# Kernel optimization log

Measured on AMD Instinct MI355X. Metric: run time of the kernel, lower is better.

## Reference

```python
import jax, jax.numpy as jnp
import numpy as np

D_MODEL = 1024
NUM_HEADS = 16
HEAD_SIZE = D_MODEL // NUM_HEADS  # 64; used ONLY as the softmax scale (module never splits heads)


def setup_inputs() -> dict:
    key = jax.random.key(0)
    ks = jax.random.split(key, 7)
    B, L, D = 4, 2048, D_MODEL
    q = jax.random.normal(ks[0], (B, L, D), dtype=jnp.float32)
    k = jax.random.normal(ks[1], (B, L, D), dtype=jnp.float32)
    v = jax.random.normal(ks[2], (B, L, D), dtype=jnp.float32)
    s = 1.0 / np.sqrt(D)
    Wq = jax.random.uniform(ks[3], (D, D), jnp.float32, -s, s)
    Wk = jax.random.uniform(ks[4], (D, D), jnp.float32, -s, s)
    Wv = jax.random.uniform(ks[5], (D, D), jnp.float32, -s, s)
    Wproj = jax.random.uniform(ks[6], (D, D), jnp.float32, -s, s)
    return {"q": q, "k": k, "v": v, "Wq": Wq, "Wk": Wk, "Wv": Wv, "Wproj": Wproj}


def reference(q, k, v, Wq, Wk, Wv, Wproj):
    # nn.Linear(x) = x @ W.T; weights stored [out, in]
    L = q.shape[1]
    qh = jnp.einsum('bld,ed->ble', q, Wq)
    kh = jnp.einsum('bld,ed->ble', k, Wk)
    vh = jnp.einsum('bld,ed->ble', v, Wv)
    # NOTE: module attends over the full d_model channel (no head split),
    # but scales by head_size ** -0.5 — faithful to the source.
    att = jnp.einsum('bqd,bkd->bqk', qh, kh) * (HEAD_SIZE ** -0.5)
    causal = jnp.tril(jnp.ones((L, L), dtype=bool))  # bias buffer
    att = jnp.where(causal, att, -jnp.inf)
    att = jax.nn.softmax(att, axis=-1)
    y = jnp.einsum('bqk,bkd->bqd', att, vh)
    y = jnp.einsum('bld,ed->ble', y, Wproj)
    return y
```

## Files before the change

kernel.cpp:

```cpp
#include <hip/hip_runtime.h>
#include <hip/hip_bf16.h>
#include <stdint.h>

typedef __bf16 bf16x8 __attribute__((ext_vector_type(8)));
typedef float  f32x4  __attribute__((ext_vector_type(4)));
typedef unsigned short ushort8v __attribute__((ext_vector_type(8)));

__device__ __forceinline__ unsigned short f2bf(float f) {
  unsigned int u = __float_as_uint(f);
  u += 0x7FFF + ((u >> 16) & 1);
  return (unsigned short)(u >> 16);
}
__device__ __forceinline__ float bf2f(unsigned short h) {
  return __uint_as_float(((unsigned int)h) << 16);
}

#define GLOAD_LDS(gptr, ldsptr)                                                     \
  __builtin_amdgcn_global_load_lds(                                                 \
      (const __attribute__((address_space(1))) unsigned int*)(gptr),                \
      (__attribute__((address_space(3))) unsigned int*)(ldsptr), 16, 0, 0)

__global__ __launch_bounds__(512, 1) void gemm8p(
    const unsigned short* __restrict__ A,
    const unsigned short* __restrict__ B,
    void* __restrict__ C,
    int M, int N, int K, int ntn,
    long sAz, long sBz, long sCz,
    int mode, int tilemap, float scale)
{
  int mt, nt;
  const int orig = blockIdx.x;
  if (tilemap == 0) {
    const int nwg = gridDim.x;
    const int qq = nwg >> 3, rr = nwg & 7, xcd = orig & 7, oo = orig >> 3;
    const int wg = (xcd < rr ? xcd * (qq + 1) : rr * (qq + 1) + (xcd - rr) * qq) + oo;
    mt = wg / ntn; nt = wg % ntn;
  } else {
    mt = (int)((sqrtf(8.f * orig + 1.f) - 1.f) * 0.5f);
    int base = mt * (mt + 1) / 2;
    if (orig < base) { mt--; base = mt * (mt + 1) / 2; }
    else if (orig >= base + mt + 1) { mt++; base = mt * (mt + 1) / 2; }
    nt = orig - base;
  }
  const int z = blockIdx.y;
  A += sAz * (long)z;
  B += sBz * (long)z;

  __shared__ __align__(16) unsigned short lds[65536];

  const int tid  = threadIdx.x;
  const int wave = tid >> 6;
  const int lane = tid & 63;
  const int wr = wave >> 2, wc = wave & 3;
  const int li = lane & 15;
  const int rslot = (((lane >> 4) ^ ((lane >> 1) & 3)) << 4);

  f32x4 acc[8][4];
#pragma unroll
  for (int i = 0; i < 8; ++i)
#pragma unroll
    for (int j = 0; j < 4; ++j) acc[i][j] = (f32x4){0.f, 0.f, 0.f, 0.f};

  const int nkt = K / 64;

  const int srow = tid >> 2;
  const long scol = (long)(((tid & 3) ^ ((tid >> 3) & 3)) << 3);
  const long aoff0 = (long)(mt * 256 + srow) * K + scol;
  const long aoff1 = (long)(mt * 256 + 128 + srow) * K + scol;
  const long boff0 = (long)(nt * 256 + srow) * K + scol;
  const long boff1 = (long)(nt * 256 + 128 + srow) * K + scol;
  const int stw = wave * 1024;

#define AB(c, kh) (((c) * 2 + (kh)) * 16384)
#define BB(c, kh) (65536 + ((c) * 2 + (kh)) * 16384)
#define STAGE_A(c, kh, jt) do { const long o_ = (long)(jt) * 64 + (kh) * 32;        \
    GLOAD_LDS(A + aoff0 + o_, (char*)lds + AB(c, kh) + stw);                        \
    GLOAD_LDS(A + aoff1 + o_, (char*)lds + AB(c, kh) + 8192 + stw); } while (0)
#define STAGE_B(c, kh, jt) do { const long o_ = (long)(jt) * 64 + (kh) * 32;        \
    GLOAD_LDS(B + boff0 + o_, (char*)lds + BB(c, kh) + stw);                        \
    GLOAD_LDS(B + boff1 + o_, (char*)lds + BB(c, kh) + 8192 + stw); } while (0)
#define RD_A(c, kk, ms, mf) \
  (*(const bf16x8*)((const char*)lds + AB(c, kk) + (wr * 128 + (ms) * 64 + (mf) * 16 + li) * 64 + rslot))
#define RD_B(c, kk, nf) \
  (*(const bf16x8*)((const char*)lds + BB(c, kk) + (wc * 64 + (nf) * 16 + li) * 64 + rslot))
#define MM(msb, bb) do {                                                            \
    _Pragma("unroll")                                                               \
    for (int mf_ = 0; mf_ < 4; ++mf_)                                               \
    _Pragma("unroll")                                                               \
      for (int nf_ = 0; nf_ < 4; ++nf_)                                             \
        acc[(msb) + mf_][nf_] = __builtin_amdgcn_mfma_f32_16x16x32_bf16(            \
            a[mf_], bb[nf_], acc[(msb) + mf_][nf_], 0, 0, 0); } while (0)
#define LGKM0_FENCE do {                                                            \
    asm volatile("s_waitcnt lgkmcnt(0)" ::: "memory");                              \
    __builtin_amdgcn_sched_barrier(0); } while (0)
#define BARRIER do { __builtin_amdgcn_s_barrier();                                  \
    asm volatile("" ::: "memory"); } while (0)

  STAGE_A(0, 0, 0); STAGE_B(0, 0, 0); STAGE_A(0, 1, 0); STAGE_B(0, 1, 0);
  asm volatile("s_waitcnt vmcnt(0)" ::: "memory");
  BARRIER;

  bf16x8 a[4], b0[4], b1[4];
  for (int j = 0; j < nkt; ++j) {
    const int c = j & 1;
    const bool s1 = (j + 1 < nkt);

#pragma unroll
    for (int nf = 0; nf < 4; ++nf) b0[nf] = RD_B(c, 0, nf);
#pragma unroll
    for (int mf = 0; mf < 4; ++mf) a[mf] = RD_A(c, 0, 0, mf);
    if (s1) STAGE_A(c ^ 1, 0, j + 1);
    BARRIER;
    LGKM0_FENCE;
    __builtin_amdgcn_s_setprio(1);
    MM(0, b0);
    __builtin_amdgcn_s_setprio(0);
    BARRIER;

#pragma unroll
    for (int mf = 0; mf < 4; ++mf) a[mf] = RD_A(c, 0, 1, mf);
    if (s1) STAGE_B(c ^ 1, 0, j + 1);
    BARRIER;
    LGKM0_FENCE;
    __builtin_amdgcn_s_setprio(1);
    MM(4, b0);
    __builtin_amdgcn_s_setprio(0);
    if (s1) { asm volatile("s_waitcnt vmcnt(4)" ::: "memory"); }
    else    { asm volatile("s_waitcnt vmcnt(0)" ::: "memory"); }
    BARRIER;

#pragma unroll
    for (int nf = 0; nf < 4; ++nf) b1[nf] = RD_B(c, 1, nf);
#pragma unroll
    for (int mf = 0; mf < 4; ++mf) a[mf] = RD_A(c, 1, 0, mf);
    if (s1) STAGE_A(c ^ 1, 1, j + 1);
    BARRIER;
    LGKM0_FENCE;
    __builtin_amdgcn_s_setprio(1);
    MM(0, b1);
    __builtin_amdgcn_s_setprio(0);
    BARRIER;

#pragma unroll
    for (int mf = 0; mf < 4; ++mf) a[mf] = RD_A(c, 1, 1, mf);
    if (s1) STAGE_B(c ^ 1, 1, j + 1);
    BARRIER;
    LGKM0_FENCE;
    __builtin_amdgcn_s_setprio(1);
    MM(4, b1);
    __builtin_amdgcn_s_setprio(0);
    if (s1) { asm volatile("s_waitcnt vmcnt(4)" ::: "memory"); }
    BARRIER;
  }
#undef AB
#undef BB
#undef STAGE_A
#undef STAGE_B
#undef RD_A
#undef RD_B
#undef MM
#undef LGKM0_FENCE
#undef BARRIER

  const int rb = mt * 256 + wr * 128;
  const int cb = nt * 256 + wc * 64;
  unsigned short* Cb = (unsigned short*)C + sCz * (long)z;
#pragma unroll
  for (int mi = 0; mi < 8; ++mi)
#pragma unroll
    for (int ni = 0; ni < 4; ++ni) {
      const int row0 = rb + mi * 16 + ((lane >> 4) << 2);
      const int col  = cb + ni * 16 + (lane & 15);
#pragma unroll
      for (int jj = 0; jj < 4; ++jj)
        Cb[(long)(row0 + jj) * N + col] = f2bf(acc[mi][ni][jj] * scale);
    }
}

#define BM 128
#define BN 128
#define BK 32

__global__ __launch_bounds__(256, 3) void gemm_bt(
    const unsigned short* __restrict__ A,
    const unsigned short* __restrict__ B,
    void* __restrict__ C,
    int M, int N, int K, int ntiles,
    long sAz, long sBz, long sCz,
    int mode, int tilemap, float scale)
{
  int mt, nt;
  const int orig = blockIdx.x;
  if (tilemap == 0) {
    const int nwg = gridDim.x;
    const int qq = nwg >> 3, rr = nwg & 7, xc = orig & 7, oo = orig >> 3;
    const int wg = (xc < rr ? xc * (qq + 1) : rr * (qq + 1) + (xc - rr) * qq) + oo;
    mt = wg / ntiles; nt = wg % ntiles;
  } else {
    const int c = orig & 15;
    mt = (c & 8) ? (15 - (c & 7)) : c;
    nt = orig >> 4;
  }
  const int z = blockIdx.y;
  const int emode = (mode == 3) ? (z == 2 ? 1 : 0) : mode;

  A += sAz * (long)z;
  B += sBz * (long)z;

  __shared__ __align__(16) unsigned short As[3][BM * BK];
  __shared__ __align__(16) unsigned short Bs[3][BN * BK];

  const int tid  = threadIdx.x;
  const int wave = tid >> 6;
  const int lane = tid & 63;
  const int wr = wave >> 1, wc = wave & 1;

  f32x4 acc[4][4];
#pragma unroll
  for (int i = 0; i < 4; ++i)
#pragma unroll
    for (int j = 0; j < 4; ++j) acc[i][j] = (f32x4){0.f, 0.f, 0.f, 0.f};

  int kiters = K / BK;
  if (tilemap == 2) { const int kl = (mt + 1) * (BM / BK); if (kl < kiters) kiters = kl; }

  const int r0 = tid >> 2, s0 = tid & 3;
  const int c0 = ((s0 ^ ((r0 >> 1) & 3)) << 3);
  const int r1 = r0 + 64;
  const int c1 = ((s0 ^ ((r1 >> 1) & 3)) << 3);
  const long aoff0 = (long)(mt * BM + r0) * K + c0;
  const long aoff1 = (long)(mt * BM + r1) * K + c1;
  const long boff0 = (long)(nt * BN + r0) * K + c0;
  const long boff1 = (long)(nt * BN + r1) * K + c1;
  const unsigned ldsw = wave * 1024;

#define STAGE(bi, k0)                                                     \
  do {                                                                    \
    GLOAD_LDS(A + aoff0 + (k0), (char*)&As[bi][0]    + ldsw);             \
    GLOAD_LDS(A + aoff1 + (k0), (char*)&As[bi][2048] + ldsw);             \
    GLOAD_LDS(B + boff0 + (k0), (char*)&Bs[bi][0]    + ldsw);             \
    GLOAD_LDS(B + boff1 + (k0), (char*)&Bs[bi][2048] + ldsw);             \
  } while (0)

  STAGE(0, 0);
  if (kiters > 1) STAGE(1, BK);

  int cur = 0;
  for (int kt = 0; kt < kiters; ++kt) {
    const int rem = kiters - 1 - kt;
    if (rem >= 2) {
      int sb = cur + 2; if (sb >= 3) sb -= 3;
      STAGE(sb, (kt + 2) * BK);
      asm volatile("s_waitcnt vmcnt(8)" ::: "memory");
    } else if (rem == 1) {
      asm volatile("s_waitcnt vmcnt(4)" ::: "memory");
    } else {
      asm volatile("s_waitcnt vmcnt(0)" ::: "memory");
    }
    __builtin_amdgcn_s_barrier();
    asm volatile("" ::: "memory");

    bf16x8 af[4], bfr[4];
#pragma unroll
    for (int i = 0; i < 4; ++i) {
      const int ar = wr * 64 + i * 16 + (lane & 15);
      const int as = ((lane >> 4) ^ ((ar >> 1) & 3)) << 3;
      af[i] = *(const bf16x8*)&As[cur][ar * BK + as];
      const int br = wc * 64 + i * 16 + (lane & 15);
      const int bs = ((lane >> 4) ^ ((br >> 1) & 3)) << 3;
      bfr[i] = *(const bf16x8*)&Bs[cur][br * BK + bs];
    }
#pragma unroll
    for (int mi = 0; mi < 4; ++mi)
#pragma unroll
      for (int ni = 0; ni < 4; ++ni)
        acc[mi][ni] = __builtin_amdgcn_mfma_f32_16x16x32_bf16(af[mi], bfr[ni], acc[mi][ni], 0, 0, 0);

    asm volatile("" ::: "memory");
    __builtin_amdgcn_s_barrier();
    cur = (cur == 2) ? 0 : cur + 1;
  }
#undef STAGE

  const int rb = mt * BM + wr * 64;
  const int cb = nt * BN + wc * 64;

  if (emode == 0) {
    unsigned short* Cb = (unsigned short*)C + sCz * (long)z;
#pragma unroll
    for (int mi = 0; mi < 4; ++mi)
#pragma unroll
      for (int ni = 0; ni < 4; ++ni) {
        const int row0 = rb + mi * 16 + ((lane >> 4) << 2);
        const int col  = cb + ni * 16 + (lane & 15);
#pragma unroll
        for (int j = 0; j < 4; ++j)
          Cb[(long)(row0 + j) * N + col] = f2bf(acc[mi][ni][j] * scale);
      }
  } else if (emode == 1) {
    unsigned short* Cb = (unsigned short*)C + sCz * (long)z;
#pragma unroll
    for (int mi = 0; mi < 4; ++mi)
#pragma unroll
      for (int ni = 0; ni < 4; ++ni) {
        const int row0 = rb + mi * 16 + ((lane >> 4) << 2);
        const int col  = cb + ni * 16 + (lane & 15);
#pragma unroll
        for (int j = 0; j < 4; ++j) {
          const int row = row0 + j;
          const int b = row >> 11, l = row & 2047;
          Cb[((long)b * N + col) * 2048 + l] = f2bf(acc[mi][ni][j]);
        }
      }
  } else {
    float* Cf = (float*)C + sCz * (long)z;
#pragma unroll
    for (int mi = 0; mi < 4; ++mi)
#pragma unroll
      for (int ni = 0; ni < 4; ++ni) {
        const int row0 = rb + mi * 16 + ((lane >> 4) << 2);
        const int col  = cb + ni * 16 + (lane & 15);
#pragma unroll
        for (int j = 0; j < 4; ++j)
          Cf[(long)(row0 + j) * N + col] = acc[mi][ni][j] * scale;
      }
  }
}

__global__ __launch_bounds__(256) void softmax_causal(
    const unsigned short* __restrict__ S, unsigned short* __restrict__ P)
{
  const int r = blockIdx.x;
  const int b = r >> 11, q = r & 2047;
  const unsigned short* srow = S + ((long)b * 2048 + q) * 2048;
  unsigned short* prow = P + ((long)b * 2048 + q) * 2048;
  const int len = q + 1;
  const int lenceil = ((q >> 7) + 1) << 7;
  const int tid = threadIdx.x, lane = tid & 63, wave = tid >> 6;
  const int base = tid * 8;
  const bool active = base < lenceil;
  __shared__ float red[8];

  float vv[8];
#pragma unroll
  for (int i = 0; i < 8; ++i) vv[i] = -3.4e38f;
  if (active) {
    ushort8v xv = *(const ushort8v*)(srow + base);
#pragma unroll
    for (int i = 0; i < 8; ++i) vv[i] = bf2f(xv[i]);
  }

  float m = -3.4e38f;
#pragma unroll
  for (int i = 0; i < 8; ++i) if (base + i < len) m = fmaxf(m, vv[i]);
#pragma unroll
  for (int o = 32; o; o >>= 1) m = fmaxf(m, __shfl_xor(m, o));
  if (lane == 0) red[wave] = m;
  __syncthreads();
  m = fmaxf(fmaxf(red[0], red[1]), fmaxf(red[2], red[3]));

  float p[8], s = 0.f;
#pragma unroll
  for (int i = 0; i < 8; ++i) {
    p[i] = (base + i < len) ? __expf(vv[i] - m) : 0.f;
    s += p[i];
  }
#pragma unroll
  for (int o = 32; o; o >>= 1) s += __shfl_xor(s, o);
  if (lane == 0) red[4 + wave] = s;
  __syncthreads();
  s = (red[4] + red[5]) + (red[6] + red[7]);
  const float inv = 1.f / s;

  if (active) {
    ushort8v o16;
#pragma unroll
    for (int i = 0; i < 8; ++i) o16[i] = f2bf(p[i] * inv);
    *(ushort8v*)(prow + base) = o16;
  }
}

__global__ __launch_bounds__(256) void convert_all(
    const float* __restrict__ q, const float* __restrict__ k, const float* __restrict__ v,
    const float* __restrict__ wq, const float* __restrict__ wk,
    const float* __restrict__ wv, const float* __restrict__ wp,
    unsigned short* __restrict__ qkv, unsigned short* __restrict__ wb)
{
  const long NQ = 8192L * 1024 / 4;
  const long NW = 1024L * 1024 / 4;
  const int blk = blockIdx.x;
  const float* src; unsigned short* dst; long n; int nb, bb;
  if (blk < 1536) {
    const int s = blk >> 9;
    src = (s == 0) ? q : (s == 1) ? k : v;
    dst = qkv + (long)s * (8192L * 1024);
    n = NQ; nb = 512; bb = blk & 511;
  } else {
    const int s = (blk - 1536) >> 6;
    src = (s == 0) ? wq : (s == 1) ? wk : (s == 2) ? wv : wp;
    dst = wb + (long)s * (1024L * 1024);
    n = NW; nb = 64; bb = (blk - 1536) & 63;
  }
  for (long i = (long)bb * 256 + threadIdx.x; i < n; i += (long)nb * 256) {
    float4 x = ((const float4*)src)[i];
    ushort4 o;
    o.x = f2bf(x.x); o.y = f2bf(x.y); o.z = f2bf(x.z); o.w = f2bf(x.w);
    ((ushort4*)dst)[i] = o;
  }
}

extern "C" void kernel_launch(void* const* d_in, const int* in_sizes, int n_in,
                              void* d_out, int out_size, void* d_ws, size_t ws_size,
                              hipStream_t stream) {
  const float* q  = (const float*)d_in[0];
  const float* k  = (const float*)d_in[1];
  const float* v  = (const float*)d_in[2];
  const float* Wq = (const float*)d_in[3];
  const float* Wk = (const float*)d_in[4];
  const float* Wv = (const float*)d_in[5];
  const float* Wp = (const float*)d_in[6];
  float* out = (float*)d_out;

  const long D  = 1024;
  const long L  = 2048;
  const long ND = 8192 * D;
  const long NS = 4L * L * L;

  char* ws = (char*)d_ws;
  unsigned short* qh    = (unsigned short*)ws;
  unsigned short* kh    = qh  + ND;
  unsigned short* vhT   = kh  + ND;
  unsigned short* wbf   = vhT + ND;
  unsigned short* S     = wbf + 4L * D * D;
  unsigned short* qkvbf = S   + NS;
  unsigned short* P     = qkvbf;
  unsigned short* ybf   = P + NS;

  convert_all<<<1792, 256, 0, stream>>>(q, k, v, Wq, Wk, Wv, Wp, qkvbf, wbf);

  gemm_bt<<<dim3(512, 3), 256, 0, stream>>>(qkvbf, wbf, qh,
      8192, 1024, 1024, 8, ND, D * D, ND, 3, 0, 1.0f);

  gemm8p<<<dim3(36, 4), 512, 0, stream>>>(qh, kh, S,
      2048, 2048, 1024, 8, L * D, L * D, L * L, 0, 1, 0.125f);

  softmax_causal<<<8192, 256, 0, stream>>>(S, P);

  gemm_bt<<<dim3(128, 4), 256, 0, stream>>>(P, vhT, ybf,
      2048, 1024, 2048, 8, L * L, D * L, L * D, 0, 2, 1.0f);

  gemm_bt<<<dim3(512, 1), 256, 0, stream>>>(ybf, wbf + 3 * D * D, out,
      8192, 1024, 1024, 8, 0, 0, 0, 2, 0, 1.0f);
}
```

Baseline: 211.8 us.

## Fuse fp32-to-bf16 activation conversion into QKV projection GEMM; use 256-tile GEMM for output proj

Replaces the separate conversion pass over q/k/v activations with a projection GEMM that loads fp32 activations straight into LDS and converts them to bf16 while building MFMA fragments. Only the weights are still pre-converted. This removes one full read and write of the activations, at the cost of doubling LDS traffic for the A operand. The final output projection now uses the larger 256x256-tile gemm8p kernel, which gains an fp32 store path, in place of the 128-tile kernel.

After: 246.6 us. 1.16x slower.

```diff
diff --git a/kernel.cpp b/kernel.cpp
--- a/kernel.cpp
+++ b/kernel.cpp
@@ -19,6 +19,131 @@
   __builtin_amdgcn_global_load_lds(                                                 \
       (const __attribute__((address_space(1))) unsigned int*)(gptr),                \
       (__attribute__((address_space(3))) unsigned int*)(ldsptr), 16, 0, 0)
+
+__global__ __launch_bounds__(256, 2) void proj_f32a(
+    const float* __restrict__ Aq, const float* __restrict__ Ak, const float* __restrict__ Av,
+    const unsigned short* __restrict__ W,
+    unsigned short* __restrict__ Out)
+{
+  const int K = 1024, N = 1024;
+  const int nwg = gridDim.x, orig = blockIdx.x;
+  const int qq = nwg >> 3, rr = nwg & 7, xc = orig & 7, oo = orig >> 3;
+  const int wg = (xc < rr ? xc * (qq + 1) : rr * (qq + 1) + (xc - rr) * qq) + oo;
+  const int mt = wg >> 3, nt = wg & 7;
+  const int z = blockIdx.y;
+  const float* A = (z == 0) ? Aq : (z == 1) ? Ak : Av;
+  const unsigned short* B = W + (long)z * (1024 * 1024);
+
+  __shared__ __align__(16) float          Asf[3][128 * 32];
+  __shared__ __align__(16) unsigned short Bs[3][128 * 32];
+
+  const int tid = threadIdx.x, wave = tid >> 6, lane = tid & 63;
+  const int wr = wave >> 1, wc = wave & 1;
+
+  f32x4 acc[4][4];
+#pragma unroll
+  for (int i = 0; i < 4; ++i)
+#pragma unroll
+    for (int j = 0; j < 4; ++j) acc[i][j] = (f32x4){0.f, 0.f, 0.f, 0.f};
+
+  const int kiters = K / 32;
+
+  const int arS = tid >> 3;
+  const int asS = tid & 7;
+  const int cAS = ((asS ^ ((arS >> 1) & 7)) << 2);
+  const long aoffS = (long)(mt * 128 + arS) * K + cAS;
+  const int brS = tid >> 2, bsS = tid & 3;
+  const int cB0 = ((bsS ^ ((brS >> 1) & 3)) << 3);
+  const int cB1 = ((bsS ^ (((brS + 64) >> 1) & 3)) << 3);
+  const long boff0 = (long)(nt * 128 + brS) * K + cB0;
+  const long boff1 = (long)(nt * 128 + 64 + brS) * K + cB1;
+  const unsigned ldsw = wave * 1024;
+
+#define STAGE(bi, k0)                                                       \
+  do {                                                                      \
+    GLOAD_LDS(A + aoffS + 0 * 32 * K + (k0), (char*)&Asf[bi][0]        + ldsw); \
+    GLOAD_LDS(A + aoffS + 1 * 32 * K + (k0), (char*)&Asf[bi][32 * 32]  + ldsw); \
+    GLOAD_LDS(A + aoffS + 2 * 32 * K + (k0), (char*)&Asf[bi][64 * 32]  + ldsw); \
+    GLOAD_LDS(A + aoffS + 3 * 32 * K + (k0), (char*)&Asf[bi][96 * 32]  + ldsw); \
+    GLOAD_LDS(B + boff0 + (k0), (char*)&Bs[bi][0]    + ldsw);               \
+    GLOAD_LDS(B + boff1 + (k0), (char*)&Bs[bi][2048] + ldsw);               \
+  } while (0)
+
+  STAGE(0, 0);
+  STAGE(1, 32);
+
+  int cur = 0;
+  for (int kt = 0; kt < kiters; ++kt) {
+    const int rem = kiters - 1 - kt;
+    if (rem >= 2) {
+      int sb = cur + 2; if (sb >= 3) sb -= 3;
+      STAGE(sb, (kt + 2) * 32);
+      asm volatile("s_waitcnt vmcnt(12)" ::: "memory");
+    } else if (rem == 1) {
+      asm volatile("s_waitcnt vmcnt(6)" ::: "memory");
+    } else {
+      asm volatile("s_waitcnt vmcnt(0)" ::: "memory");
+    }
+    __builtin_amdgcn_s_barrier();
+    asm volatile("" ::: "memory");
+
+    bf16x8 af[4], bfr[4];
+#pragma unroll
+    for (int i = 0; i < 4; ++i) {
+      const int ar = wr * 64 + i * 16 + (lane & 15);
+      const int sw = (ar >> 1) & 7;
+      const int k2 = (lane >> 4) << 1;
+      const float4 lo = *(const float4*)&Asf[cur][ar * 32 + (((k2)     ^ sw) << 2)];
+      const float4 hi = *(const float4*)&Asf[cur][ar * 32 + (((k2 + 1) ^ sw) << 2)];
+      af[i] = (bf16x8){(__bf16)lo.x, (__bf16)lo.y, (__bf16)lo.z, (__bf16)lo.w,
+                       (__bf16)hi.x, (__bf16)hi.y, (__bf16)hi.z, (__bf16)hi.w};
+      const int br = wc * 64 + i * 16 + (lane & 15);
+      const int bs = ((lane >> 4) ^ ((br >> 1) & 3)) << 3;
+      bfr[i] = *(const bf16x8*)&Bs[cur][br * 32 + bs];
+    }
+#pragma unroll
+    for (int mi = 0; mi < 4; ++mi)
+#pragma unroll
+      for (int ni = 0; ni < 4; ++ni)
+        acc[mi][ni] = __builtin_amdgcn_mfma_f32_16x16x32_bf16(af[mi], bfr[ni], acc[mi][ni], 0, 0, 0);
+
+    asm volatile("" ::: "memory");
+    __builtin_amdgcn_s_barrier();
+    cur = (cur == 2) ? 0 : cur + 1;
+  }
+#undef STAGE
+
+  const int rb = mt * 128 + wr * 64;
+  const int cb = nt * 128 + wc * 64;
+  if (z < 2) {
+    unsigned short* Cb = Out + (long)z * (8192L * 1024);
+#pragma unroll
+    for (int mi = 0; mi < 4; ++mi)
+#pragma unroll
+      for (int ni = 0; ni < 4; ++ni) {
+        const int row0 = rb + mi * 16 + ((lane >> 4) << 2);
+        const int col  = cb + ni * 16 + (lane & 15);
+#pragma unroll
+        for (int j = 0; j < 4; ++j)
+          Cb[(long)(row0 + j) * N + col] = f2bf(acc[mi][ni][j]);
+      }
+  } else {
+    unsigned short* Cb = Out + 2L * (8192L * 1024);
+#pragma unroll
+    for (int mi = 0; mi < 4; ++mi)
+#pragma unroll
+      for (int ni = 0; ni < 4; ++ni) {
+        const int row0 = rb + mi * 16 + ((lane >> 4) << 2);
+        const int col  = cb + ni * 16 + (lane & 15);
+#pragma unroll
+        for (int j = 0; j < 4; ++j) {
+          const int row = row0 + j;
+          const int b = row >> 11, l = row & 2047;
+          Cb[((long)b * N + col) * 2048 + l] = f2bf(acc[mi][ni][j]);
+        }
+      }
+  }
+}
 
 __global__ __launch_bounds__(512, 1) void gemm8p(
     const unsigned short* __restrict__ A,
@@ -164,17 +289,31 @@
 
   const int rb = mt * 256 + wr * 128;
   const int cb = nt * 256 + wc * 64;
-  unsigned short* Cb = (unsigned short*)C + sCz * (long)z;
-#pragma unroll
-  for (int mi = 0; mi < 8; ++mi)
-#pragma unroll
-    for (int ni = 0; ni < 4; ++ni) {
-      const int row0 = rb + mi * 16 + ((lane >> 4) << 2);
-      const int col  = cb + ni * 16 + (lane & 15);
-#pragma unroll
-      for (int jj = 0; jj < 4; ++jj)
-        Cb[(long)(row0 + jj) * N + col] = f2bf(acc[mi][ni][jj] * scale);
-    }
+  if (mode == 2) {
+    float* Cf = (float*)C + sCz * (long)z;
+#pragma unroll
+    for (int mi = 0; mi < 8; ++mi)
+#pragma unroll
+      for (int ni = 0; ni < 4; ++ni) {
+        const int row0 = rb + mi * 16 + ((lane >> 4) << 2);
+        const int col  = cb + ni * 16 + (lane & 15);
+#pragma unroll
+        for (int jj = 0; jj < 4; ++jj)
+          Cf[(long)(row0 + jj) * N + col] = acc[mi][ni][jj] * scale;
+      }
+  } else {
+    unsigned short* Cb = (unsigned short*)C + sCz * (long)z;
+#pragma unroll
+    for (int mi = 0; mi < 8; ++mi)
+#pragma unroll
+      for (int ni = 0; ni < 4; ++ni) {
+        const int row0 = rb + mi * 16 + ((lane >> 4) << 2);
+        const int col  = cb + ni * 16 + (lane & 15);
+#pragma unroll
+        for (int jj = 0; jj < 4; ++jj)
+          Cb[(long)(row0 + jj) * N + col] = f2bf(acc[mi][ni][jj] * scale);
+      }
+  }
 }
 
 #define BM 128
@@ -202,7 +341,6 @@
     nt = orig >> 4;
   }
   const int z = blockIdx.y;
-  const int emode = (mode == 3) ? (z == 2 ? 1 : 0) : mode;
 
   A += sAz * (long)z;
   B += sBz * (long)z;
@@ -284,47 +422,17 @@
 
   const int rb = mt * BM + wr * 64;
   const int cb = nt * BN + wc * 64;
-
-  if (emode == 0) {
-    unsigned short* Cb = (unsigned short*)C + sCz * (long)z;
-#pragma unroll
-    for (int mi = 0; mi < 4; ++mi)
-#pragma unroll
-      for (int ni = 0; ni < 4; ++ni) {
-        const int row0 = rb + mi * 16 + ((lane >> 4) << 2);
-        const int col  = cb + ni * 16 + (lane & 15);
-#pragma unroll
-        for (int j = 0; j < 4; ++j)
-          Cb[(long)(row0 + j) * N + col] = f2bf(acc[mi][ni][j] * scale);
-      }
-  } else if (emode == 1) {
-    unsigned short* Cb = (unsigned short*)C + sCz * (long)z;
-#pragma unroll
-    for (int mi = 0; mi < 4; ++mi)
-#pragma unroll
-      for (int ni = 0; ni < 4; ++ni) {
-        const int row0 = rb + mi * 16 + ((lane >> 4) << 2);
-        const int col  = cb + ni * 16 + (lane & 15);
-#pragma unroll
-        for (int j = 0; j < 4; ++j) {
-          const int row = row0 + j;
-          const int b = row >> 11, l = row & 2047;
-          Cb[((long)b * N + col) * 2048 + l] = f2bf(acc[mi][ni][j]);
-        }
-      }
-  } else {
-    float* Cf = (float*)C + sCz * (long)z;
-#pragma unroll
-    for (int mi = 0; mi < 4; ++mi)
-#pragma unroll
-      for (int ni = 0; ni < 4; ++ni) {
-        const int row0 = rb + mi * 16 + ((lane >> 4) << 2);
-        const int col  = cb + ni * 16 + (lane & 15);
-#pragma unroll
-        for (int j = 0; j < 4; ++j)
-          Cf[(long)(row0 + j) * N + col] = acc[mi][ni][j] * scale;
-      }
-  }
+  unsigned short* Cb = (unsigned short*)C + sCz * (long)z;
+#pragma unroll
+  for (int mi = 0; mi < 4; ++mi)
+#pragma unroll
+    for (int ni = 0; ni < 4; ++ni) {
+      const int row0 = rb + mi * 16 + ((lane >> 4) << 2);
+      const int col  = cb + ni * 16 + (lane & 15);
+#pragma unroll
+      for (int j = 0; j < 4; ++j)
+        Cb[(long)(row0 + j) * N + col] = f2bf(acc[mi][ni][j] * scale);
+    }
 }
 
 __global__ __launch_bounds__(256) void softmax_causal(
@@ -380,32 +488,21 @@
   }
 }
 
-__global__ __launch_bounds__(256) void convert_all(
-    const float* __restrict__ q, const float* __restrict__ k, const float* __restrict__ v,
+__global__ __launch_bounds__(256) void convert_w(
     const float* __restrict__ wq, const float* __restrict__ wk,
     const float* __restrict__ wv, const float* __restrict__ wp,
-    unsigned short* __restrict__ qkv, unsigned short* __restrict__ wb)
+    unsigned short* __restrict__ wb)
 {
-  const long NQ = 8192L * 1024 / 4;
-  const long NW = 1024L * 1024 / 4;
-  const int blk = blockIdx.x;
-  const float* src; unsigned short* dst; long n; int nb, bb;
-  if (blk < 1536) {
-    const int s = blk >> 9;
-    src = (s == 0) ? q : (s == 1) ? k : v;
-    dst = qkv + (long)s * (8192L * 1024);
-    n = NQ; nb = 512; bb = blk & 511;
-  } else {
-    const int s = (blk - 1536) >> 6;
-    src = (s == 0) ? wq : (s == 1) ? wk : (s == 2) ? wv : wp;
-    dst = wb + (long)s * (1024L * 1024);
-    n = NW; nb = 64; bb = (blk - 1536) & 63;
-  }
-  for (long i = (long)bb * 256 + threadIdx.x; i < n; i += (long)nb * 256) {
-    float4 x = ((const float4*)src)[i];
+  const long NV = 262144;
+  for (long i = (long)blockIdx.x * 256 + threadIdx.x; i < 4 * NV;
+       i += (long)gridDim.x * 256) {
+    const int seg = (int)(i >> 18);
+    const long off = i & (NV - 1);
+    const float* src = (seg == 0) ? wq : (seg == 1) ? wk : (seg == 2) ? wv : wp;
+    float4 x = ((const float4*)src)[off];
     ushort4 o;
     o.x = f2bf(x.x); o.y = f2bf(x.y); o.z = f2bf(x.z); o.w = f2bf(x.w);
-    ((ushort4*)dst)[i] = o;
+    ((ushort4*)(wb + (long)seg * 1048576))[off] = o;
   }
 }
 
@@ -427,19 +524,17 @@
   const long NS = 4L * L * L;
 
   char* ws = (char*)d_ws;
-  unsigned short* qh    = (unsigned short*)ws;
-  unsigned short* kh    = qh  + ND;
-  unsigned short* vhT   = kh  + ND;
-  unsigned short* wbf   = vhT + ND;
-  unsigned short* S     = wbf + 4L * D * D;
-  unsigned short* qkvbf = S   + NS;
-  unsigned short* P     = qkvbf;
-  unsigned short* ybf   = P + NS;
-
-  convert_all<<<1792, 256, 0, stream>>>(q, k, v, Wq, Wk, Wv, Wp, qkvbf, wbf);
-
-  gemm_bt<<<dim3(512, 3), 256, 0, stream>>>(qkvbf, wbf, qh,
-      8192, 1024, 1024, 8, ND, D * D, ND, 3, 0, 1.0f);
+  unsigned short* qh  = (unsigned short*)ws;
+  unsigned short* kh  = qh  + ND;
+  unsigned short* vhT = kh  + ND;
+  unsigned short* wbf = vhT + ND;
+  unsigned short* S   = wbf + 4L * D * D;
+  unsigned short* P   = S   + NS;
+  unsigned short* ybf = P   + NS;
+
+  convert_w<<<1024, 256, 0, stream>>>(Wq, Wk, Wv, Wp, wbf);
+
+  proj_f32a<<<dim3(512, 3), 256, 0, stream>>>(q, k, v, wbf, qh);
 
   gemm8p<<<dim3(36, 4), 512, 0, stream>>>(qh, kh, S,
       2048, 2048, 1024, 8, L * D, L * D, L * L, 0, 1, 0.125f);
@@ -449,6 +544,6 @@
   gemm_bt<<<dim3(128, 4), 256, 0, stream>>>(P, vhT, ybf,
       2048, 1024, 2048, 8, L * L, D * L, L * D, 0, 2, 1.0f);
 
-  gemm_bt<<<dim3(512, 1), 256, 0, stream>>>(ybf, wbf + 3 * D * D, out,
-      8192, 1024, 1024, 8, 0, 0, 0, 2, 0, 1.0f);
-}
+  gemm8p<<<dim3(128, 1), 512, 0, stream>>>(ybf, wbf + 3 * D * D, out,
+      8192, 1024, 1024, 4, 0, 0, 0, 2, 0, 1.0f);
+}
```
